# Kernel optimization log

Measured on AMD Instinct MI355X. Metric: run time of the kernel, lower is better.

Reference implementation:

```python
import jax, jax.numpy as jnp
import numpy as np

KS = 7  # neighborhood kernel size

def _wn(v, g):
    # weight-normalized 1x1-conv weight: v [out,in], g [out]
    n = jnp.sqrt(jnp.sum(v * v, axis=1, keepdims=True))
    return v * (g[:, None] / n)

def _ln(x, gamma, beta, eps=1e-6):
    mu = jnp.mean(x, axis=-1, keepdims=True)
    var = jnp.mean(jnp.square(x - mu), axis=-1, keepdims=True)
    return (x - mu) * jax.lax.rsqrt(var + eps) * gamma + beta

def _up_nearest(c, H, W):
    # integer-factor nearest upsample on channels-last [B,h,w,C]
    rh, rw = H // c.shape[1], W // c.shape[2]
    return jnp.repeat(jnp.repeat(c, rh, axis=1), rw, axis=2)

def _adaln(x, cond, gamma, beta, v, g):
    xn = _ln(x, gamma, beta)
    cu = _up_nearest(jax.nn.silu(cond), x.shape[1], x.shape[2])
    ab = cu @ _wn(v, g).T
    a, b = jnp.split(ab, 2, axis=-1)
    return xn * (1.0 + a) + b

def _gate(x, cond, v, g):
    cu = _up_nearest(jax.nn.silu(cond), x.shape[1], x.shape[2])
    return x * (cu @ _wn(v, g).T)

def _neigh_idx(n, k):
    # NATTEN-style clamped window starts: each query sees exactly k in-bounds neighbors
    starts = np.clip(np.arange(n) - k // 2, 0, n - k)
    return jnp.asarray(starts[:, None] + np.arange(k))  # [n,k]

def _natten2d(x, w_qkv, b_qkv, w_out, b_out, n_heads):
    B, H, W, C = x.shape
    hd = C // n_heads
    qkv = x @ w_qkv.T + b_qkv
    q, k, v = jnp.split(qkv, 3, axis=-1)
    q = q.reshape(B, H, W, n_heads, hd)
    k = k.reshape(B, H, W, n_heads, hd)
    v = v.reshape(B, H, W, n_heads, hd)
    ih = _neigh_idx(H, KS)
    iw = _neigh_idx(W, KS)
    def gather(t):
        t = t[:, ih]            # [B,H,KS,W,nh,hd]
        t = t[:, :, :, iw]      # [B,H,KS,W,KS,nh,hd]
        t = jnp.transpose(t, (0, 1, 3, 5, 2, 4, 6))  # [B,H,W,nh,KS,KS,hd]
        return t.reshape(B, H, W, n_heads, KS * KS, hd)
    kn, vn = gather(k), gather(v)
    scale = jnp.asarray(1.0 / np.sqrt(hd), x.dtype)
    logits = jnp.einsum('bhwnd,bhwnkd->bhwnk', q, kn) * scale
    attn = jax.nn.softmax(logits, axis=-1)
    out = jnp.einsum('bhwnk,bhwnkd->bhwnd', attn, vn).reshape(B, H, W, C)
    return out @ w_out.T + b_out

def _mlp(x, w1, b1, w2, b2):
    return jax.nn.gelu(x @ w1.T + b1) @ w2.T + b2

def setup_inputs():
    key = jax.random.key(0)
    B, H, W, D, CD, NH = 2, 48, 48, 384, 384, 6
    ks = jax.random.split(key, 10)
    s = 0.02
    return dict(
        x=jax.random.normal(ks[0], (B, H, W, D), jnp.float32),
        cond=jax.random.normal(ks[1], (B, 6, 6, CD), jnp.float32),
        ln1_g=jnp.ones((D,), jnp.float32), ln1_b=jnp.zeros((D,), jnp.float32),
        ada1_v=jax.random.normal(ks[2], (2 * D, CD), jnp.float32) * s,
        ada1_g=jnp.ones((2 * D,), jnp.float32),
        ln2_g=jnp.ones((D,), jnp.float32), ln2_b=jnp.zeros((D,), jnp.float32),
        ada2_v=jax.random.normal(ks[3], (2 * D, CD), jnp.float32) * s,
        ada2_g=jnp.ones((2 * D,), jnp.float32),
        gate1_v=jax.random.normal(ks[4], (D, CD), jnp.float32) * s,
        gate1_g=jnp.ones((D,), jnp.float32),
        gate2_v=jax.random.normal(ks[5], (D, CD), jnp.float32) * s,
        gate2_g=jnp.ones((D,), jnp.float32),
        w_qkv=jax.random.normal(ks[6], (3 * D, D), jnp.float32) * s,
        b_qkv=jnp.zeros((3 * D,), jnp.float32),
        w_out=jax.random.normal(ks[7], (D, D), jnp.float32) * s,
        b_out=jnp.zeros((D,), jnp.float32),
        w_mlp1=jax.random.normal(ks[8], (4 * D, D), jnp.float32) * s,
        b_mlp1=jnp.zeros((4 * D,), jnp.float32),
        w_mlp2=jax.random.normal(ks[9], (D, 4 * D), jnp.float32) * s,
        b_mlp2=jnp.zeros((D,), jnp.float32),
        n_heads=NH,
    )

def reference(x, cond, ln1_g, ln1_b, ada1_v, ada1_g, ln2_g, ln2_b, ada2_v, ada2_g,
              gate1_v, gate1_g, gate2_v, gate2_g, w_qkv, b_qkv, w_out, b_out,
              w_mlp1, b_mlp1, w_mlp2, b_mlp2, n_heads):
    h = _adaln(x, cond, ln1_g, ln1_b, ada1_v, ada1_g)
    h = _natten2d(h, w_qkv, b_qkv, w_out, b_out, n_heads)
    h = _gate(h, cond, gate1_v, gate1_g)
    x = x + h
    h = _adaln(x, cond, ln2_g, ln2_b, ada2_v, ada2_g)
    h = _mlp(h, w_mlp1, b_mlp1, w_mlp2, b_mlp2)
    h = _gate(h, cond, gate2_v, gate2_g)
    return x + h
```

## Files before the change

### kernel.cpp

```cpp
#include <hip/hip_runtime.h>
#include <hip/hip_bf16.h>
#include <math.h>

#define NPIX 4608
#define D 384
#define CD 384
#define C3 1152
#define DMLP 1536
#define NCELL 72

typedef unsigned short u16;
typedef __attribute__((ext_vector_type(8))) short bf16x8;
typedef __attribute__((ext_vector_type(4))) float f32x4;

#define OFF_MOD   0
#define OFF_BIG   663552
#define OFF_HHI   28975104
#define OFF_HLO   32514048
#define OFF_AHI   36052992
#define OFF_ALO   39591936
#define OFF_MHI   43130880
#define OFF_MLO   57286656
#define OFF_WHI   71442432
#define OFF_WLO   74981376
#define BIGOFF_MODV_HI  0
#define BIGOFF_MODV_LO  1769472
#define BIGOFF_SC_HI    3538944
#define BIGOFF_SC_LO    3637248
#define BIGOFF_INVN     3735552
#define WOFF_QKV  0
#define WOFF_OUT  442368
#define WOFF_M1   589824
#define WOFF_M2   1179648

#define GLOAD16(g, l) __builtin_amdgcn_global_load_lds( \
    (const __attribute__((address_space(1))) unsigned int*)(g), \
    (__attribute__((address_space(3))) unsigned int*)(l), 16, 0, 0)

__device__ __forceinline__ float wsum(float v) {
    #pragma unroll
    for (int o = 32; o > 0; o >>= 1) v += __shfl_xor(v, o);
    return v;
}
__device__ __forceinline__ void split_bf16(float x, u16& h, u16& l) {
    __hip_bfloat16 bh = __float2bfloat16(x);
    float fh = __bfloat162float(bh);
    __hip_bfloat16 bl = __float2bfloat16(x - fh);
    h = *(u16*)&bh; l = *(u16*)&bl;
}

__global__ __launch_bounds__(256) void wconv_kernel(
    const float* __restrict__ wq, const float* __restrict__ wo,
    const float* __restrict__ w1, const float* __restrict__ w2,
    const float* __restrict__ a1v, const float* __restrict__ a2v,
    const float* __restrict__ g1v, const float* __restrict__ g2v,
    u16* __restrict__ whi, u16* __restrict__ wlo,
    u16* __restrict__ mvhi, u16* __restrict__ mvlo)
{
    int i4 = blockIdx.x * 256 + threadIdx.x;
    const float* src; int l4; u16 *dh, *dl; int o;
    if (i4 < 442368) {
        if (i4 < 110592)        { src = wq; l4 = i4; }
        else if (i4 < 147456)   { src = wo; l4 = i4 - 110592; }
        else if (i4 < 294912)   { src = w1; l4 = i4 - 147456; }
        else                    { src = w2; l4 = i4 - 294912; }
        dh = whi; dl = wlo; o = i4 * 4;
    } else {
        int j4 = i4 - 442368;
        if (j4 < 73728)         { src = a1v; l4 = j4; }
        else if (j4 < 147456)   { src = a2v; l4 = j4 - 73728; }
        else if (j4 < 184320)   { src = g1v; l4 = j4 - 147456; }
        else                    { src = g2v; l4 = j4 - 184320; }
        dh = mvhi; dl = mvlo; o = j4 * 4;
    }
    float4 v = ((const float4*)src)[l4];
    split_bf16(v.x, dh[o+0], dl[o+0]);
    split_bf16(v.y, dh[o+1], dl[o+1]);
    split_bf16(v.z, dh[o+2], dl[o+2]);
    split_bf16(v.w, dh[o+3], dl[o+3]);
}

__global__ __launch_bounds__(256) void modprep_kernel(
    const float* __restrict__ cond,
    const float* __restrict__ a1v, const float* __restrict__ a1g,
    const float* __restrict__ a2v, const float* __restrict__ a2g,
    const float* __restrict__ g1v, const float* __restrict__ g1g,
    const float* __restrict__ g2v, const float* __restrict__ g2g,
    float* __restrict__ invn, u16* __restrict__ schi, u16* __restrict__ sclo)
{
    int wid  = (blockIdx.x * blockDim.x + threadIdx.x) >> 6;
    int lane = threadIdx.x & 63;
    if (wid < 2304) {
        const float* V; float g; int r;
        if (wid < 768)        { r = wid;        V = a1v; g = a1g[r]; }
        else if (wid < 1536)  { r = wid - 768;  V = a2v; g = a2g[r]; }
        else if (wid < 1920)  { r = wid - 1536; V = g1v; g = g1g[r]; }
        else                  { r = wid - 1920; V = g2v; g = g2g[r]; }
        const float* vrow = V + r * CD;
        float nrm = 0.f;
        #pragma unroll
        for (int j = 0; j < 6; j++) {
            float v = vrow[lane + 64 * j];
            nrm += v * v;
        }
        nrm = wsum(nrm);
        if (lane == 0) invn[wid] = g / sqrtf(nrm);
    } else {
        int cell = wid - 2304;
        #pragma unroll
        for (int j = 0; j < 6; j++) {
            int k = lane + 64 * j;
            float val = 0.f;
            if (cell < NCELL) {
                float c = cond[cell * CD + k];
                val = c / (1.f + __expf(-c));
            }
            split_bf16(val, schi[cell * CD + k], sclo[cell * CD + k]);
        }
    }
}

__global__ __launch_bounds__(256) void modgemm_mfma(
    const u16* __restrict__ Ah, const u16* __restrict__ Al,
    const u16* __restrict__ Bh, const u16* __restrict__ Bl,
    const float* __restrict__ invn, float* __restrict__ mod)
{
    __shared__ u16 lds[24576];
    const int tid  = threadIdx.x;
    const int lane = tid & 63;
    const int wid  = tid >> 6;
    const int n0 = blockIdx.x * 64;
    const int K = 384, nt = 12;
    const int wr = wid >> 1, wc = wid & 1;

    const u16* gsrc[6];
    int loff[6];
    #pragma unroll
    for (int s = 0; s < 6; s++) {
        int c = tid + (s << 8);
        const u16* base; int ks, row;
        if (c < 512)        { ks = c >> 7;           row = c & 127; base = Ah + (size_t)row * K; }
        else if (c < 1024)  { int cc = c - 512;  ks = cc >> 7; row = cc & 127; base = Al + (size_t)row * K; }
        else if (c < 1280)  { int cc = c - 1024; ks = cc >> 6; row = cc & 63;  base = Bh + (size_t)(n0 + row) * K; }
        else                { int cc = c - 1280; ks = cc >> 6; row = cc & 63;  base = Bl + (size_t)(n0 + row) * K; }
        gsrc[s] = base + ks * 8;
        loff[s] = c * 8;
    }

    f32x4 acc[4][2] = {};
    const int ks = lane >> 4;
    const int fr = lane & 15;

    #pragma unroll
    for (int s = 0; s < 6; s++) GLOAD16(gsrc[s], &lds[loff[s]]);
    __syncthreads();

    int cur = 0;
    for (int kt = 0; kt < nt; kt++) {
        if (kt + 1 < nt) {
            int k0 = (kt + 1) << 5;
            int dbo = (cur ^ 1) * 12288;
            #pragma unroll
            for (int s = 0; s < 6; s++) GLOAD16(gsrc[s] + k0, &lds[dbo + loff[s]]);
        }
        const int b0 = cur * 12288;
        bf16x8 ah[4], al[4], bh[2], bl[2];
        #pragma unroll
        for (int m = 0; m < 4; m++) {
            int ai = b0 + (ks * 128 + wr * 64 + m * 16 + fr) * 8;
            ah[m] = *(const bf16x8*)&lds[ai];
            al[m] = *(const bf16x8*)&lds[4096 + ai];
        }
        #pragma unroll
        for (int n = 0; n < 2; n++) {
            int bi = b0 + (ks * 64 + wc * 32 + n * 16 + fr) * 8;
            bh[n] = *(const bf16x8*)&lds[8192 + bi];
            bl[n] = *(const bf16x8*)&lds[10240 + bi];
        }
        #pragma unroll
        for (int m = 0; m < 4; m++)
            #pragma unroll
            for (int n = 0; n < 2; n++) {
                acc[m][n] = __builtin_amdgcn_mfma_f32_16x16x32_bf16(ah[m], bh[n], acc[m][n], 0, 0, 0);
                acc[m][n] = __builtin_amdgcn_mfma_f32_16x16x32_bf16(ah[m], bl[n], acc[m][n], 0, 0, 0);
                acc[m][n] = __builtin_amdgcn_mfma_f32_16x16x32_bf16(al[m], bh[n], acc[m][n], 0, 0, 0);
            }
        __syncthreads();
        cur ^= 1;
    }

    const int r4 = ks * 4;
    #pragma unroll
    for (int m = 0; m < 4; m++) {
        #pragma unroll
        for (int n = 0; n < 2; n++) {
            #pragma unroll
            for (int j = 0; j < 4; j++) {
                int row = wr * 64 + m * 16 + r4 + j;
                int col = n0 + wc * 32 + n * 16 + fr;
                if (row < NCELL)
                    mod[(size_t)row * 2304 + col] = acc[m][n][j] * invn[col];
            }
        }
    }
}

__global__ __launch_bounds__(256) void adaln_kernel(
    const float* __restrict__ x,
    const float* __restrict__ gamma, const float* __restrict__ beta,
    const float* __restrict__ mod_ab,
    u16* __restrict__ ohi, u16* __restrict__ olo)
{
    int p    = (blockIdx.x * blockDim.x + threadIdx.x) >> 6;
    int lane = threadIdx.x & 63;
    int b  = p / 2304;
    int hh = (p / 48) % 48;
    int ww = p % 48;
    int cell = b * 36 + (hh >> 3) * 6 + (ww >> 3);

    const float* xr = x + (size_t)p * D;
    float v[6]; float s = 0.f, ss = 0.f;
    #pragma unroll
    for (int j = 0; j < 6; j++) {
        v[j] = xr[lane + 64 * j];
        s  += v[j];
        ss += v[j] * v[j];
    }
    s = wsum(s); ss = wsum(ss);
    float mu  = s * (1.f / 384.f);
    float var = ss * (1.f / 384.f) - mu * mu;
    float rs  = 1.f / sqrtf(var + 1e-6f);

    const float* ab = mod_ab + (size_t)cell * 2304;
    #pragma unroll
    for (int j = 0; j < 6; j++) {
        int d = lane + 64 * j;
        float xn = (v[j] - mu) * rs * gamma[d] + beta[d];
        float o  = xn * (1.f + ab[d]) + ab[384 + d];
        split_bf16(o, ohi[(size_t)p * D + d], olo[(size_t)p * D + d]);
    }
}

template <int EPI>
__global__ __launch_bounds__(256) void gemm_mfma(
    const u16* __restrict__ Ah, const u16* __restrict__ Al,
    const u16* __restrict__ Bh, const u16* __restrict__ Bl,
    const float* __restrict__ bias,
    float* __restrict__ Cf, u16* __restrict__ Ch, u16* __restrict__ Cl,
    const float* __restrict__ gate, const float* __restrict__ resid,
    int N, int K)
{
    __shared__ u16 lds[24576];
    const int tid  = threadIdx.x;
    const int lane = tid & 63;
    const int wid  = tid >> 6;

    const int nwg = gridDim.x;
    const int q = nwg >> 3, r = nwg & 7;
    const int xcd = blockIdx.x & 7, loc = blockIdx.x >> 3;
    const int wgid = (xcd < r ? xcd * (q + 1) : r * (q + 1) + (xcd - r) * q) + loc;

    const int nx = N >> 6;
    const int by = wgid / nx;
    const int bx = wgid - by * nx;
    const int m0 = by * 64;
    const int n0 = bx * 64;
    const int nt = K >> 5;

    const int wr = wid >> 1, wc = wid & 1;

    const u16* gsrc[4];
    int loff[4];
    #pragma unroll
    for (int s = 0; s < 4; s++) {
        int c = tid + (s << 8);
        int ks = (c & 255) >> 6;
        int row = c & 63;
        const u16* base;
        if (c < 256)       base = Ah + (size_t)(m0 + row) * K;
        else if (c < 512)  base = Al + (size_t)(m0 + row) * K;
        else if (c < 768)  base = Bh + (size_t)(n0 + row) * K;
        else               base = Bl + (size_t)(n0 + row) * K;
        gsrc[s] = base + ks * 8;
        loff[s] = c * 8;
    }

    f32x4 acc[2][2] = {};
    const int ks = lane >> 4;
    const int fr = lane & 15;

    #pragma unroll
    for (int s = 0; s < 4; s++) GLOAD16(gsrc[s], &lds[loff[s]]);
    #pragma unroll
    for (int s = 0; s < 4; s++) GLOAD16(gsrc[s] + 32, &lds[8192 + loff[s]]);

    for (int kt = 0; kt < nt; kt++) {
        if (kt + 2 < nt) {
            int k0 = (kt + 2) << 5;
            int dbo = ((kt + 2) % 3) * 8192;
            #pragma unroll
            for (int s = 0; s < 4; s++) GLOAD16(gsrc[s] + k0, &lds[dbo + loff[s]]);
        }
        int rem = nt - 1 - kt;
        if (rem >= 2)      asm volatile("s_waitcnt vmcnt(8)" ::: "memory");
        else if (rem == 1) asm volatile("s_waitcnt vmcnt(4)" ::: "memory");
        else               asm volatile("s_waitcnt vmcnt(0)" ::: "memory");
        __builtin_amdgcn_s_barrier();

        const int b0 = (kt % 3) * 8192;
        bf16x8 ah[2], al[2], bh[2], bl[2];
        #pragma unroll
        for (int m = 0; m < 2; m++) {
            int ai = b0 + (ks * 64 + wr * 32 + m * 16 + fr) * 8;
            ah[m] = *(const bf16x8*)&lds[ai];
            al[m] = *(const bf16x8*)&lds[2048 + ai];
        }
        #pragma unroll
        for (int n = 0; n < 2; n++) {
            int bi = b0 + (ks * 64 + wc * 32 + n * 16 + fr) * 8;
            bh[n] = *(const bf16x8*)&lds[4096 + bi];
            bl[n] = *(const bf16x8*)&lds[6144 + bi];
        }
        asm volatile("s_waitcnt lgkmcnt(0)" ::: "memory");
        __builtin_amdgcn_sched_barrier(0);
        __builtin_amdgcn_s_barrier();

        #pragma unroll
        for (int m = 0; m < 2; m++)
            #pragma unroll
            for (int n = 0; n < 2; n++) {
                acc[m][n] = __builtin_amdgcn_mfma_f32_16x16x32_bf16(ah[m], bh[n], acc[m][n], 0, 0, 0);
                acc[m][n] = __builtin_amdgcn_mfma_f32_16x16x32_bf16(ah[m], bl[n], acc[m][n], 0, 0, 0);
                acc[m][n] = __builtin_amdgcn_mfma_f32_16x16x32_bf16(al[m], bh[n], acc[m][n], 0, 0, 0);
            }
    }

    const int r4 = ks * 4;
    #pragma unroll
    for (int m = 0; m < 2; m++) {
        #pragma unroll
        for (int n = 0; n < 2; n++) {
            #pragma unroll
            for (int j = 0; j < 4; j++) {
                int row = m0 + wr * 32 + m * 16 + r4 + j;
                int col = n0 + wc * 32 + n * 16 + fr;
                float v = acc[m][n][j];
                if (EPI == 0) {
                    Cf[(size_t)row * N + col] = v + bias[col];
                } else if (EPI == 1) {
                    float t = v + bias[col];
                    float c = 0.7978845608028654f * (t + 0.044715f * t * t * t);
                    float e = __expf(2.f * c);
                    float th = (e - 1.f) / (e + 1.f);
                    float g = 0.5f * t * (1.f + th);
                    size_t idx = (size_t)row * N + col;
                    split_bf16(g, Ch[idx], Cl[idx]);
                } else {
                    int b  = row / 2304;
                    int hh = (row / 48) % 48;
                    int ww = row % 48;
                    int cell = b * 36 + (hh >> 3) * 6 + (ww >> 3);
                    size_t idx = (size_t)row * N + col;
                    Cf[idx] = resid[idx] + (v + bias[col]) * gate[(size_t)cell * 2304 + col];
                }
            }
        }
    }
}

__global__ __launch_bounds__(256) void natten_kernel(
    const float* __restrict__ qkv, u16* __restrict__ ohi, u16* __restrict__ olo)
{
    const int nwg = gridDim.x;
    const int q8 = nwg >> 3, r8 = nwg & 7;
    const int xcd = blockIdx.x & 7, loc = blockIdx.x >> 3;
    const int bswz = (xcd < r8 ? xcd * (q8 + 1) : r8 * (q8 + 1) + (xcd - r8) * q8) + loc;

    int wid  = bswz * 4 + (threadIdx.x >> 6);
    int lane = threadIdx.x & 63;
    int head = wid % 6;
    int p    = wid / 6;
    int b  = p / 2304;
    int hh = (p / 48) % 48;
    int ww = p % 48;
    int sh = hh - 3; sh = sh < 0 ? 0 : (sh > 41 ? 41 : sh);
    int sw = ww - 3; sw = sw < 0 ? 0 : (sw > 41 ? 41 : sw);
    int pb = b * 2304;

    const int n_sub = lane >> 3;
    const int d_sub = lane & 7;
    const int dof = head * 64 + d_sub * 8;

    int npo[7];
    #pragma unroll
    for (int t = 0; t < 7; t++) {
        int n = t * 8 + n_sub;
        int nn = n > 48 ? 48 : n;
        int nr = nn / 7, nc = nn - nr * 7;
        npo[t] = pb + (sh + nr) * 48 + (sw + nc);
    }

    const float* qp = qkv + (size_t)p * C3 + dof;
    float4 q0 = *(const float4*)qp;
    float4 q1 = *(const float4*)(qp + 4);
    q0.x *= 0.125f; q0.y *= 0.125f; q0.z *= 0.125f; q0.w *= 0.125f;
    q1.x *= 0.125f; q1.y *= 0.125f; q1.z *= 0.125f; q1.w *= 0.125f;

    float4 kk0[7], kk1[7];
    #pragma unroll
    for (int t = 0; t < 7; t++) {
        const float* kp = qkv + (size_t)npo[t] * C3 + 384 + dof;
        kk0[t] = *(const float4*)kp;
        kk1[t] = *(const float4*)(kp + 4);
    }
    __builtin_amdgcn_sched_barrier(0);

    float L[7];
    #pragma unroll
    for (int t = 0; t < 7; t++) {
        float d = q0.x * kk0[t].x + q0.y * kk0[t].y + q0.z * kk0[t].z + q0.w * kk0[t].w
                + q1.x * kk1[t].x + q1.y * kk1[t].y + q1.z * kk1[t].z + q1.w * kk1[t].w;
        d += __shfl_xor(d, 1);
        d += __shfl_xor(d, 2);
        d += __shfl_xor(d, 4);
        L[t] = (t * 8 + n_sub < 49) ? d : -INFINITY;
    }

    float4 vv0[7], vv1[7];
    #pragma unroll
    for (int t = 0; t < 7; t++) {
        const float* vp = qkv + (size_t)npo[t] * C3 + 768 + dof;
        vv0[t] = *(const float4*)vp;
        vv1[t] = *(const float4*)(vp + 4);
    }
    __builtin_amdgcn_sched_barrier(0);

    float m = L[0];
    #pragma unroll
    for (int t = 1; t < 7; t++) m = fmaxf(m, L[t]);
    m = fmaxf(m, __shfl_xor(m, 8));
    m = fmaxf(m, __shfl_xor(m, 16));
    m = fmaxf(m, __shfl_xor(m, 32));

    float w[7]; float s = 0.f;
    #pragma unroll
    for (int t = 0; t < 7; t++) {
        w[t] = (L[t] == -INFINITY) ? 0.f : __expf(L[t] - m);
        s += w[t];
    }
    s += __shfl_xor(s, 8);
    s += __shfl_xor(s, 16);
    s += __shfl_xor(s, 32);
    float inv = 1.f / s;
    #pragma unroll
    for (int t = 0; t < 7; t++) w[t] *= inv;

    float a0x = 0.f, a0y = 0.f, a0z = 0.f, a0w = 0.f;
    float a1x = 0.f, a1y = 0.f, a1z = 0.f, a1w = 0.f;
    #pragma unroll
    for (int t = 0; t < 7; t++) {
        float wn = w[t];
        a0x = fmaf(wn, vv0[t].x, a0x); a0y = fmaf(wn, vv0[t].y, a0y);
        a0z = fmaf(wn, vv0[t].z, a0z); a0w = fmaf(wn, vv0[t].w, a0w);
        a1x = fmaf(wn, vv1[t].x, a1x); a1y = fmaf(wn, vv1[t].y, a1y);
        a1z = fmaf(wn, vv1[t].z, a1z); a1w = fmaf(wn, vv1[t].w, a1w);
    }
    #pragma unroll
    for (int o = 8; o <= 32; o <<= 1) {
        a0x += __shfl_xor(a0x, o); a0y += __shfl_xor(a0y, o);
        a0z += __shfl_xor(a0z, o); a0w += __shfl_xor(a0w, o);
        a1x += __shfl_xor(a1x, o); a1y += __shfl_xor(a1y, o);
        a1z += __shfl_xor(a1z, o); a1w += __shfl_xor(a1w, o);
    }

    if (lane < 8) {
        float av[8] = {a0x, a0y, a0z, a0w, a1x, a1y, a1z, a1w};
        u16 hi8[8], lo8[8];
        #pragma unroll
        for (int i = 0; i < 8; i++) split_bf16(av[i], hi8[i], lo8[i]);
        size_t oi = (size_t)p * D + head * 64 + lane * 8;
        *(uint4*)(ohi + oi) = *(uint4*)hi8;
        *(uint4*)(olo + oi) = *(uint4*)lo8;
    }
}

extern "C" void kernel_launch(void* const* d_in, const int* in_sizes, int n_in,
                              void* d_out, int out_size, void* d_ws, size_t ws_size,
                              hipStream_t stream)
{
    (void)in_sizes; (void)n_in; (void)out_size; (void)ws_size;
    const float* x      = (const float*)d_in[0];
    const float* cond   = (const float*)d_in[1];
    const float* ln1_g  = (const float*)d_in[2];
    const float* ln1_b  = (const float*)d_in[3];
    const float* ada1_v = (const float*)d_in[4];
    const float* ada1_g = (const float*)d_in[5];
    const float* ln2_g  = (const float*)d_in[6];
    const float* ln2_b  = (const float*)d_in[7];
    const float* ada2_v = (const float*)d_in[8];
    const float* ada2_g = (const float*)d_in[9];
    const float* gate1_v = (const float*)d_in[10];
    const float* gate1_g = (const float*)d_in[11];
    const float* gate2_v = (const float*)d_in[12];
    const float* gate2_g = (const float*)d_in[13];
    const float* w_qkv  = (const float*)d_in[14];
    const float* b_qkv  = (const float*)d_in[15];
    const float* w_out  = (const float*)d_in[16];
    const float* b_out  = (const float*)d_in[17];
    const float* w_mlp1 = (const float*)d_in[18];
    const float* b_mlp1 = (const float*)d_in[19];
    const float* w_mlp2 = (const float*)d_in[20];
    const float* b_mlp2 = (const float*)d_in[21];

    char* ws = (char*)d_ws;
    float* mod  = (float*)(ws + OFF_MOD);
    float* big  = (float*)(ws + OFF_BIG);
    u16* h_hi   = (u16*)(ws + OFF_HHI);
    u16* h_lo   = (u16*)(ws + OFF_HLO);
    u16* a_hi   = (u16*)(ws + OFF_AHI);
    u16* a_lo   = (u16*)(ws + OFF_ALO);
    u16* m_hi   = (u16*)(ws + OFF_MHI);
    u16* m_lo   = (u16*)(ws + OFF_MLO);
    u16* w_hi   = (u16*)(ws + OFF_WHI);
    u16* w_lo   = (u16*)(ws + OFF_WLO);
    char* bigc  = ws + OFF_BIG;
    u16* mv_hi  = (u16*)(bigc + BIGOFF_MODV_HI);
    u16* mv_lo  = (u16*)(bigc + BIGOFF_MODV_LO);
    u16* sc_hi  = (u16*)(bigc + BIGOFF_SC_HI);
    u16* sc_lo  = (u16*)(bigc + BIGOFF_SC_LO);
    float* invn = (float*)(bigc + BIGOFF_INVN);
    float* x2   = (float*)d_out;

    wconv_kernel<<<2592, 256, 0, stream>>>(
        w_qkv, w_out, w_mlp1, w_mlp2, ada1_v, ada2_v, gate1_v, gate2_v,
        w_hi, w_lo, mv_hi, mv_lo);

    modprep_kernel<<<608, 256, 0, stream>>>(
        cond, ada1_v, ada1_g, ada2_v, ada2_g, gate1_v, gate1_g, gate2_v, gate2_g,
        invn, sc_hi, sc_lo);

    modgemm_mfma<<<36, 256, 0, stream>>>(sc_hi, sc_lo, mv_hi, mv_lo, invn, mod);

    adaln_kernel<<<NPIX / 4, 256, 0, stream>>>(x, ln1_g, ln1_b, mod, h_hi, h_lo);

    gemm_mfma<0><<<1296, 256, 0, stream>>>(
        h_hi, h_lo, w_hi + WOFF_QKV, w_lo + WOFF_QKV, b_qkv,
        big, nullptr, nullptr, nullptr, nullptr, C3, D);

    natten_kernel<<<(NPIX * 6) / 4, 256, 0, stream>>>(big, a_hi, a_lo);

    gemm_mfma<3><<<432, 256, 0, stream>>>(
        a_hi, a_lo, w_hi + WOFF_OUT, w_lo + WOFF_OUT, b_out,
        x2, nullptr, nullptr, mod + 1536, x, D, D);

    adaln_kernel<<<NPIX / 4, 256, 0, stream>>>(x2, ln2_g, ln2_b, mod + 768, h_hi, h_lo);

    gemm_mfma<1><<<1728, 256, 0, stream>>>(
        h_hi, h_lo, w_hi + WOFF_M1, w_lo + WOFF_M1, b_mlp1,
        nullptr, m_hi, m_lo, nullptr, nullptr, DMLP, D);

    gemm_mfma<3><<<432, 256, 0, stream>>>(
        m_hi, m_lo, w_hi + WOFF_M2, w_lo + WOFF_M2, b_mlp2,
        x2, nullptr, nullptr, mod + 1920, x2, D, DMLP);
}
```

Before: 323.9 us.

## Use 8 waves per GEMM tile and deepen LDS pipeline to four stages

The split-bf16 MFMA GEMM now runs 512 threads per 64x64 tile, with each wave computing a 16x32 sub-tile instead of 32x32. Global-to-LDS prefetch goes from three buffers to four, with adjusted vmcnt waits. The aim is more waves in flight to hide memory latency and a deeper prefetch. In exchange, each wave reuses fewer A/B fragments per LDS read, LDS use per block rises, and barriers must now synchronise twice as many waves.

```diff
diff --git a/kernel.cpp b/kernel.cpp
--- a/kernel.cpp
+++ b/kernel.cpp
@@ -242,7 +242,7 @@
 }
 
 template <int EPI>
-__global__ __launch_bounds__(256) void gemm_mfma(
+__global__ __launch_bounds__(512) void gemm_mfma(
     const u16* __restrict__ Ah, const u16* __restrict__ Al,
     const u16* __restrict__ Bh, const u16* __restrict__ Bl,
     const float* __restrict__ bias,
@@ -250,7 +250,7 @@
     const float* __restrict__ gate, const float* __restrict__ resid,
     int N, int K)
 {
-    __shared__ u16 lds[24576];
+    __shared__ u16 lds[32768];
     const int tid  = threadIdx.x;
     const int lane = tid & 63;
     const int wid  = tid >> 6;
@@ -267,13 +267,14 @@
     const int n0 = bx * 64;
     const int nt = K >> 5;
 
-    const int wr = wid >> 1, wc = wid & 1;
-
-    const u16* gsrc[4];
-    int loff[4];
-    #pragma unroll
-    for (int s = 0; s < 4; s++) {
-        int c = tid + (s << 8);
+    const int wr = wid >> 1;
+    const int wc = wid & 1;
+
+    const u16* gsrc[2];
+    int loff[2];
+    #pragma unroll
+    for (int s = 0; s < 2; s++) {
+        int c = tid + (s << 9);
         int ks = (c & 255) >> 6;
         int row = c & 63;
         const u16* base;
@@ -285,84 +286,81 @@
         loff[s] = c * 8;
     }
 
-    f32x4 acc[2][2] = {};
+    f32x4 acc[2] = {};
     const int ks = lane >> 4;
     const int fr = lane & 15;
 
     #pragma unroll
-    for (int s = 0; s < 4; s++) GLOAD16(gsrc[s], &lds[loff[s]]);
-    #pragma unroll
-    for (int s = 0; s < 4; s++) GLOAD16(gsrc[s] + 32, &lds[8192 + loff[s]]);
+    for (int s = 0; s < 2; s++) GLOAD16(gsrc[s],      &lds[loff[s]]);
+    #pragma unroll
+    for (int s = 0; s < 2; s++) GLOAD16(gsrc[s] + 32, &lds[8192 + loff[s]]);
+    #pragma unroll
+    for (int s = 0; s < 2; s++) GLOAD16(gsrc[s] + 64, &lds[16384 + loff[s]]);
 
     for (int kt = 0; kt < nt; kt++) {
-        if (kt + 2 < nt) {
-            int k0 = (kt + 2) << 5;
-            int dbo = ((kt + 2) % 3) * 8192;
+        if (kt + 3 < nt) {
+            int k0 = (kt + 3) << 5;
+            int dbo = ((kt + 3) & 3) * 8192;
             #pragma unroll
-            for (int s = 0; s < 4; s++) GLOAD16(gsrc[s] + k0, &lds[dbo + loff[s]]);
+            for (int s = 0; s < 2; s++) GLOAD16(gsrc[s] + k0, &lds[dbo + loff[s]]);
         }
         int rem = nt - 1 - kt;
-        if (rem >= 2)      asm volatile("s_waitcnt vmcnt(8)" ::: "memory");
-        else if (rem == 1) asm volatile("s_waitcnt vmcnt(4)" ::: "memory");
+        if (rem >= 3)      asm volatile("s_waitcnt vmcnt(6)" ::: "memory");
+        else if (rem == 2) asm volatile("s_waitcnt vmcnt(4)" ::: "memory");
+        else if (rem == 1) asm volatile("s_waitcnt vmcnt(2)" ::: "memory");
         else               asm volatile("s_waitcnt vmcnt(0)" ::: "memory");
         __builtin_amdgcn_s_barrier();
 
-        const int b0 = (kt % 3) * 8192;
-        bf16x8 ah[2], al[2], bh[2], bl[2];
-        #pragma unroll
-        for (int m = 0; m < 2; m++) {
-            int ai = b0 + (ks * 64 + wr * 32 + m * 16 + fr) * 8;
-            ah[m] = *(const bf16x8*)&lds[ai];
-            al[m] = *(const bf16x8*)&lds[2048 + ai];
+        const int b0 = (kt & 3) * 8192;
+        bf16x8 ah, al, bh[2], bl[2];
+        {
+            int ai = b0 + (ks * 64 + wr * 16 + fr) * 8;
+            ah = *(const bf16x8*)&lds[ai];
+            al = *(const bf16x8*)&lds[2048 + ai];
         }
         #pragma unroll
         for (int n = 0; n < 2; n++) {
-            int bi = b0 + (ks * 64 + wc * 32 + n * 16 + fr) * 8;
-            bh[n] = *(const bf16x8*)&lds[4096 + bi];
-            bl[n] = *(const bf16x8*)&lds[6144 + bi];
+            int bi = b0 + 4096 + (ks * 64 + wc * 32 + n * 16 + fr) * 8;
+            bh[n] = *(const bf16x8*)&lds[bi];
+            bl[n] = *(const bf16x8*)&lds[2048 + bi];
         }
         asm volatile("s_waitcnt lgkmcnt(0)" ::: "memory");
         __builtin_amdgcn_sched_barrier(0);
         __builtin_amdgcn_s_barrier();
 
         #pragma unroll
-        for (int m = 0; m < 2; m++)
-            #pragma unroll
-            for (int n = 0; n < 2; n++) {
-                acc[m][n] = __builtin_amdgcn_mfma_f32_16x16x32_bf16(ah[m], bh[n], acc[m][n], 0, 0, 0);
-                acc[m][n] = __builtin_amdgcn_mfma_f32_16x16x32_bf16(ah[m], bl[n], acc[m][n], 0, 0, 0);
-                acc[m][n] = __builtin_amdgcn_mfma_f32_16x16x32_bf16(al[m], bh[n], acc[m][n], 0, 0, 0);
-            }
+        for (int n = 0; n < 2; n++) {
+            acc[n] = __builtin_amdgcn_mfma_f32_16x16x32_bf16(ah, bh[n], acc[n], 0, 0, 0);
+            acc[n] = __builtin_amdgcn_mfma_f32_16x16x32_bf16(ah, bl[n], acc[n], 0, 0, 0);
+            acc[n] = __builtin_amdgcn_mfma_f32_16x16x32_bf16(al, bh[n], acc[n], 0, 0, 0);
+        }
     }
 
     const int r4 = ks * 4;
     #pragma unroll
-    for (int m = 0; m < 2; m++) {
-        #pragma unroll
-        for (int n = 0; n < 2; n++) {
-            #pragma unroll
-            for (int j = 0; j < 4; j++) {
-                int row = m0 + wr * 32 + m * 16 + r4 + j;
-                int col = n0 + wc * 32 + n * 16 + fr;
-                float v = acc[m][n][j];
-                if (EPI == 0) {
-                    Cf[(size_t)row * N + col] = v + bias[col];
-                } else if (EPI == 1) {
-                    float t = v + bias[col];
-                    float c = 0.7978845608028654f * (t + 0.044715f * t * t * t);
-                    float e = __expf(2.f * c);
-                    float th = (e - 1.f) / (e + 1.f);
-                    float g = 0.5f * t * (1.f + th);
-                    size_t idx = (size_t)row * N + col;
-                    split_bf16(g, Ch[idx], Cl[idx]);
-                } else {
-                    int b  = row / 2304;
-                    int hh = (row / 48) % 48;
-                    int ww = row % 48;
-                    int cell = b * 36 + (hh >> 3) * 6 + (ww >> 3);
-                    size_t idx = (size_t)row * N + col;
-                    Cf[idx] = resid[idx] + (v + bias[col]) * gate[(size_t)cell * 2304 + col];
-                }
+    for (int n = 0; n < 2; n++) {
+        #pragma unroll
+        for (int j = 0; j < 4; j++) {
+            int row = m0 + wr * 16 + r4 + j;
+            int col = n0 + wc * 32 + n * 16 + fr;
+            float v = acc[n][j];
+            if (EPI == 0) {
+                Cf[(size_t)row * N + col] = v + bias[col];
+            } else if (EPI == 1) {
+                float t = v + bias[col];
+                float c = 0.7978845608028654f * (t + 0.044715f * t * t * t);
+                float e = __expf(2.f * c);
+                float th = (e - 1.f) / (e + 1.f);
+                float g = 0.5f * t * (1.f + th);
+                size_t idx = (size_t)row * N + col;
+                split_bf16(g, Ch[idx], Cl[idx]);
+            } else {
+                int b  = row / 2304;
+                int hh = (row / 48) % 48;
+                int ww = row % 48;
+                int cell = b * 36 + (hh >> 3) * 6 + (ww >> 3);
+                size_t idx = (size_t)row * N + col;
+                Cf[idx] = resid[idx] + (v + bias[col]) * gate[(size_t)cell * 2304 + col];
             }
         }
     }
@@ -543,23 +541,23 @@
 
     adaln_kernel<<<NPIX / 4, 256, 0, stream>>>(x, ln1_g, ln1_b, mod, h_hi, h_lo);
 
-    gemm_mfma<0><<<1296, 256, 0, stream>>>(
+    gemm_mfma<0><<<1296, 512, 0, stream>>>(
         h_hi, h_lo, w_hi + WOFF_QKV, w_lo + WOFF_QKV, b_qkv,
         big, nullptr, nullptr, nullptr, nullptr, C3, D);
 
     natten_kernel<<<(NPIX * 6) / 4, 256, 0, stream>>>(big, a_hi, a_lo);
 
-    gemm_mfma<3><<<432, 256, 0, stream>>>(
+    gemm_mfma<3><<<432, 512, 0, stream>>>(
         a_hi, a_lo, w_hi + WOFF_OUT, w_lo + WOFF_OUT, b_out,
         x2, nullptr, nullptr, mod + 1536, x, D, D);
 
     adaln_kernel<<<NPIX / 4, 256, 0, stream>>>(x2, ln2_g, ln2_b, mod + 768, h_hi, h_lo);
 
-    gemm_mfma<1><<<1728, 256, 0, stream>>>(
+    gemm_mfma<1><<<1728, 512, 0, stream>>>(
         h_hi, h_lo, w_hi + WOFF_M1, w_lo + WOFF_M1, b_mlp1,
         nullptr, m_hi, m_lo, nullptr, nullptr, DMLP, D);
 
-    gemm_mfma<3><<<432, 256, 0, stream>>>(
+    gemm_mfma<3><<<432, 512, 0, stream>>>(
         m_hi, m_lo, w_hi + WOFF_M2, w_lo + WOFF_M2, b_mlp2,
         x2, nullptr, nullptr, mod + 1920, x2, D, DMLP);
 }
```

After: 319.7 us. Within noise of the previous version (-1.3%).
